# Optimization experiments

Measured on AMD Instinct MI355X. Metric: run time of the kernel, lower is better.

Reference implementation:

```python
import jax, jax.numpy as jnp
import numpy as np
from jax import lax

B, S, N, DIM = 4, 512, 16, 8
D_MODEL, D_STATE = 1024, 64
INPUT_SIZE = N * DIM
LN_EPS = 1e-5


def setup_inputs() -> dict:
    key = jax.random.key(0)
    ks = jax.random.split(key, 8)
    s = 0.02
    x = jax.random.normal(ks[0], (B, S, N, DIM), dtype=jnp.float32)
    W_emb = jax.random.normal(ks[1], (INPUT_SIZE, D_MODEL), dtype=jnp.float32) * s
    b_emb = jnp.zeros((D_MODEL,), jnp.float32)
    W_xp = jax.random.normal(ks[2], (D_MODEL, 2 * D_STATE + 1), dtype=jnp.float32) * s
    b_xp = jnp.zeros((2 * D_STATE + 1,), jnp.float32)
    # A init: -exp(arange(1, d_state+1) * 0.1), matching the torch module
    A = -jnp.exp(jnp.arange(1, D_STATE + 1, dtype=jnp.float32) * 0.1)
    Dp = jnp.ones((D_MODEL,), jnp.float32)
    gamma = jnp.ones((D_MODEL,), jnp.float32)
    beta = jnp.zeros((D_MODEL,), jnp.float32)
    W_out = jax.random.normal(ks[3], (D_MODEL, INPUT_SIZE), dtype=jnp.float32) * s
    b_out = jnp.zeros((INPUT_SIZE,), jnp.float32)
    return {"x": x, "W_emb": W_emb, "b_emb": b_emb, "W_xp": W_xp, "b_xp": b_xp,
            "A": A, "Dp": Dp, "gamma": gamma, "beta": beta,
            "W_out": W_out, "b_out": b_out}


def reference(x, W_emb, b_emb, W_xp, b_xp, A, Dp, gamma, beta, W_out, b_out):
    b, s, n, dim = x.shape
    d_state = A.shape[0]
    d_model = W_emb.shape[1]
    u = x.reshape(b, s, n * dim) @ W_emb + b_emb            # [B,S,dm]
    sel = u @ W_xp + b_xp                                    # [B,S,2*ds+1]
    delta = jax.nn.softplus(sel[..., 0:1]) * 0.01            # [B,S,1]
    Bs = sel[..., 1:1 + d_state]                             # [B,S,ds]
    Cs = sel[..., 1 + d_state:]                              # [B,S,ds]
    A_bar = jnp.exp(delta * A)                               # [B,S,ds]
    B_bar = delta * Bs                                       # [B,S,ds]

    def step(h, inp):
        a_t, b_t, c_t, u_t = inp                             # [B,ds],[B,ds],[B,ds],[B,dm]
        h = h * a_t[:, None, :] + b_t[:, None, :] * u_t[:, :, None]  # [B,dm,ds]
        y_t = jnp.einsum('bmd,bd->bm', h, c_t) + u_t * Dp
        return h, y_t

    h0 = jnp.zeros((b, d_model, d_state), x.dtype)
    xs = (jnp.swapaxes(A_bar, 0, 1), jnp.swapaxes(B_bar, 0, 1),
          jnp.swapaxes(Cs, 0, 1), jnp.swapaxes(u, 0, 1))
    _, ys = lax.scan(step, h0, xs)                           # ys: [S,B,dm]
    y = jnp.swapaxes(ys, 0, 1)                               # [B,S,dm]
    mu = y.mean(-1, keepdims=True)
    var = y.var(-1, keepdims=True)
    yn = (y - mu) / jnp.sqrt(var + LN_EPS) * gamma + beta
    pred = yn @ W_out + b_out                                # [B,S,N*D]
    return pred.reshape(b, s, n, dim)
```

## Files before the change

kernel.cpp:

```cpp
#include <hip/hip_runtime.h>
#include <cstddef>

typedef __attribute__((ext_vector_type(8))) short short8;
typedef __attribute__((ext_vector_type(4))) float f32x4;

constexpr int CL = 32;

__device__ inline ushort tobf(float f) {
  union { float f; unsigned u; } v; v.f = f;
  return (ushort)((v.u + 0x7FFFu + ((v.u >> 16) & 1u)) >> 16);
}
__device__ inline float frombf(ushort u) {
  union { unsigned u; float f; } v; v.u = ((unsigned)u) << 16; return v.f;
}

__global__ __launch_bounds__(256)
void prep(const float* __restrict__ Wemb, const float* __restrict__ Wxp,
          const float* __restrict__ Wout, const float* __restrict__ x,
          const float* __restrict__ bxp, const float* __restrict__ bout,
          ushort* __restrict__ WembT, ushort* __restrict__ wBCdT,
          ushort* __restrict__ WoutT, ushort* __restrict__ xbf,
          float* __restrict__ sel, float* __restrict__ sums,
          float* __restrict__ out) {
  int idx = blockIdx.x * 256 + threadIdx.x;
  if (idx < 131072) {
    int n = idx >> 7, k = idx & 127;
    WembT[idx] = tobf(Wemb[k * 1024 + n]);
  } else if (idx < 327680) {
    int j = idx - 131072;
    int n = j >> 10, k = j & 1023;
    float v = (n < 128) ? Wxp[k * 129 + 1 + n] : (n == 128 ? Wxp[k * 129] : 0.f);
    wBCdT[j] = tobf(v);
  } else if (idx < 458752) {
    int j = idx - 327680;
    int n = j >> 10, k = j & 1023;
    WoutT[j] = tobf(Wout[k * 128 + n]);
  } else if (idx < 720896) {
    int j = idx - 458752;
    xbf[j] = tobf(x[j]);
  } else if (idx < 1114112) {
    int j = idx - 720896;
    int c = j % 192;
    sel[j] = (c < 128) ? bxp[1 + c] : (c == 128 ? bxp[0] : 0.f);
  } else if (idx < 1118208) {
    sums[idx - 1114112] = 0.f;
  } else if (idx < 1380352) {
    int j = idx - 1118208;
    out[j] = bout[j & 127];
  }
}

template<int MODE>
__global__ __launch_bounds__(256)
void gemm_bt(const ushort* __restrict__ A, const ushort* __restrict__ BT,
             const float* __restrict__ bias, float* __restrict__ Cf,
             ushort* __restrict__ Cbf, int M, int N, int K, int kchunk) {
  __shared__ __align__(16) ushort sA[8192];
  __shared__ __align__(16) ushort sB[8192];
  const int t  = threadIdx.x;
  const int n0 = blockIdx.x * 64;
  const int m0 = blockIdx.y * 64;
  const int k0 = (MODE == 1) ? blockIdx.z * kchunk : 0;
  const int k1 = (MODE == 1) ? k0 + kchunk : K;

  const int lane = t & 63, w = t >> 6;
  const int wr = w << 4;
  const int colsel = lane & 15;
  const int kg = lane >> 4;

  f32x4 acc[4];
  #pragma unroll
  for (int nf = 0; nf < 4; ++nf) acc[nf] = (f32x4)(0.f);

  for (int kc = k0; kc < k1; kc += 128) {
    __syncthreads();
    #pragma unroll
    for (int i = 0; i < 4; ++i) {
      int c = t + (i << 8);
      int row = c >> 4, kk = (c & 15) << 3;
      float4 va  = *(const float4*)(A  + (size_t)(m0 + row) * K + kc + kk);
      float4 vb4 = *(const float4*)(BT + (size_t)(n0 + row) * K + kc + kk);
      int byteoff = ((row << 8) + (kk << 1)) ^ ((row & 7) << 4);
      *(float4*)((char*)sA + byteoff) = va;
      *(float4*)((char*)sB + byteoff) = vb4;
    }
    __syncthreads();
    short8 a[4];
    {
      int arow = wr + colsel;
      int lin = (arow << 8) + (kg << 4);
      int swz = (arow & 7) << 4;
      #pragma unroll
      for (int ks = 0; ks < 4; ++ks)
        a[ks] = *(const short8*)((const char*)sA + ((lin + (ks << 6)) ^ swz));
    }
    #pragma unroll
    for (int nf = 0; nf < 4; ++nf) {
      int brow = (nf << 4) + colsel;
      int lin = (brow << 8) + (kg << 4);
      int swz = (brow & 7) << 4;
      #pragma unroll
      for (int ks = 0; ks < 4; ++ks) {
        short8 b = *(const short8*)((const char*)sB + ((lin + (ks << 6)) ^ swz));
        acc[nf] = __builtin_amdgcn_mfma_f32_16x16x32_bf16(a[ks], b, acc[nf], 0, 0, 0);
      }
    }
  }
  const int r4 = kg << 2;
  #pragma unroll
  for (int nf = 0; nf < 4; ++nf) {
    int gn = n0 + (nf << 4) + colsel;
    #pragma unroll
    for (int reg = 0; reg < 4; ++reg) {
      int gm = m0 + wr + r4 + reg;
      if (MODE == 0) {
        Cbf[(size_t)gm * N + gn] = tobf(acc[nf][reg] + bias[gn]);
      } else {
        atomicAdd(&Cf[(size_t)gm * N + gn], acc[nf][reg]);
      }
    }
  }
}

__global__ __launch_bounds__(256)
void gemm_ln(const ushort* __restrict__ ybf, const ushort* __restrict__ BT,
             const float* __restrict__ sums, const float* __restrict__ gamma,
             const float* __restrict__ beta, float* __restrict__ out) {
  __shared__ __align__(16) ushort sA[8192];
  __shared__ __align__(16) ushort sB[8192];
  __shared__ float sLN[128];
  const int t  = threadIdx.x;
  const int n0 = blockIdx.x * 64;
  const int m0 = blockIdx.y * 64;
  const int k0 = blockIdx.z * 256;
  const int k1 = k0 + 256;

  if (t < 64) {
    float s1 = sums[m0 + t], s2 = sums[2048 + m0 + t];
    float mean = s1 * (1.f / 1024.f);
    float var  = s2 * (1.f / 1024.f) - mean * mean;
    sLN[2 * t] = mean;
    sLN[2 * t + 1] = rsqrtf(var + 1e-5f);
  }

  const int lane = t & 63, w = t >> 6;
  const int wr = w << 4;
  const int colsel = lane & 15;
  const int kg = lane >> 4;
  const int kk_t = (t & 15) << 3;

  f32x4 acc[4];
  #pragma unroll
  for (int nf = 0; nf < 4; ++nf) acc[nf] = (f32x4)(0.f);

  for (int kc = k0; kc < k1; kc += 128) {
    float4 g0 = *(const float4*)&gamma[kc + kk_t];
    float4 g1 = *(const float4*)&gamma[kc + kk_t + 4];
    float4 be0 = *(const float4*)&beta[kc + kk_t];
    float4 be1 = *(const float4*)&beta[kc + kk_t + 4];
    float gv[8] = {g0.x, g0.y, g0.z, g0.w, g1.x, g1.y, g1.z, g1.w};
    float bv[8] = {be0.x, be0.y, be0.z, be0.w, be1.x, be1.y, be1.z, be1.w};
    __syncthreads();
    #pragma unroll
    for (int i = 0; i < 4; ++i) {
      int c = t + (i << 8);
      int row = c >> 4, kk = (c & 15) << 3;
      short8 ya = *(const short8*)(ybf + (size_t)(m0 + row) * 1024 + kc + kk);
      float4 vb4 = *(const float4*)(BT + (size_t)(n0 + row) * 1024 + kc + kk);
      float mean = sLN[2 * row], rstd = sLN[2 * row + 1];
      short8 na;
      #pragma unroll
      for (int j = 0; j < 8; ++j) {
        float yv = frombf((ushort)ya[j]);
        na[j] = (short)tobf((yv - mean) * rstd * gv[j] + bv[j]);
      }
      int byteoff = ((row << 8) + (kk << 1)) ^ ((row & 7) << 4);
      *(short8*)((char*)sA + byteoff) = na;
      *(float4*)((char*)sB + byteoff) = vb4;
    }
    __syncthreads();
    short8 a[4];
    {
      int arow = wr + colsel;
      int lin = (arow << 8) + (kg << 4);
      int swz = (arow & 7) << 4;
      #pragma unroll
      for (int ks = 0; ks < 4; ++ks)
        a[ks] = *(const short8*)((const char*)sA + ((lin + (ks << 6)) ^ swz));
    }
    #pragma unroll
    for (int nf = 0; nf < 4; ++nf) {
      int brow = (nf << 4) + colsel;
      int lin = (brow << 8) + (kg << 4);
      int swz = (brow & 7) << 4;
      #pragma unroll
      for (int ks = 0; ks < 4; ++ks) {
        short8 b = *(const short8*)((const char*)sB + ((lin + (ks << 6)) ^ swz));
        acc[nf] = __builtin_amdgcn_mfma_f32_16x16x32_bf16(a[ks], b, acc[nf], 0, 0, 0);
      }
    }
  }
  const int r4 = kg << 2;
  #pragma unroll
  for (int nf = 0; nf < 4; ++nf) {
    int gn = n0 + (nf << 4) + colsel;
    #pragma unroll
    for (int reg = 0; reg < 4; ++reg) {
      int gm = m0 + wr + r4 + reg;
      atomicAdd(&out[(size_t)gm * 128 + gn], acc[nf][reg]);
    }
  }
}

__device__ __forceinline__ void transform_sbuf(float* sbuf, float a_d, int t) {
  const int d = t & 63;
  #pragma unroll
  for (int i = 0; i < 8; ++i) {
    float* R = sbuf + ((t >> 6) + i * 4) * 192;
    float draw = R[128];
    float sp = (draw > 15.f) ? draw : log1pf(__expf(draw));
    float delta = 0.01f * sp;
    R[d] = delta * R[d];
    R[128 + d] = __expf(delta * a_d);
  }
}

__global__ __launch_bounds__(256)
void scan_sum(const ushort* __restrict__ ubf, const float* __restrict__ sel,
              const float* __restrict__ A,
              float* __restrict__ cst, float* __restrict__ Ach) {
  __shared__ __align__(16) float sbuf[CL * 192];
  const int t = threadIdx.x, lane = t & 63, w = t >> 6;
  const int tc = blockIdx.x % 15;
  const int mg = (blockIdx.x / 15) & 3;
  const int b  = blockIdx.x / 60;
  const int r0 = b * 512 + tc * CL;

  const float a_d = A[t & 63];
  const float4* src = (const float4*)(sel + (size_t)r0 * 192);
  #pragma unroll
  for (int i = 0; i < 6; ++i)
    ((float4*)sbuf)[t + i * 256] = src[t + i * 256];
  __syncthreads();
  transform_sbuf(sbuf, a_d, t);
  __syncthreads();

  const int m = (mg * 4 + w) * 64 + lane;
  const ushort* ub = ubf + (size_t)r0 * 1024 + m;
  const bool doAp = (mg == 0 && w == 0);

  float2 h[32], ap[32];
  #pragma unroll
  for (int j = 0; j < 32; ++j) { h[j] = make_float2(0.f, 0.f); ap[j] = make_float2(1.f, 1.f); }

  float u0 = frombf(ub[0]);
  float u1 = frombf(ub[1024]);
  for (int s = 0; s < CL; ++s) {
    int sn = (s < CL - 3) ? s + 2 : CL - 1;
    float u2 = frombf(ub[(size_t)sn * 1024]);
    const float* L = sbuf + s * 192;
    #pragma unroll
    for (int jj = 0; jj < 16; ++jj) {
      float4 a4 = *(const float4*)&L[128 + 4 * jj];
      float4 b4 = *(const float4*)&L[4 * jj];
      h[2 * jj].x     = fmaf(h[2 * jj].x,     a4.x, b4.x * u0);
      h[2 * jj].y     = fmaf(h[2 * jj].y,     a4.y, b4.y * u0);
      h[2 * jj + 1].x = fmaf(h[2 * jj + 1].x, a4.z, b4.z * u0);
      h[2 * jj + 1].y = fmaf(h[2 * jj + 1].y, a4.w, b4.w * u0);
    }
    if (doAp) {
      #pragma unroll
      for (int jj = 0; jj < 16; ++jj) {
        float4 a4 = *(const float4*)&L[128 + 4 * jj];
        ap[2 * jj].x     *= a4.x;
        ap[2 * jj].y     *= a4.y;
        ap[2 * jj + 1].x *= a4.z;
        ap[2 * jj + 1].y *= a4.w;
      }
    }
    u0 = u1; u1 = u2;
  }

  size_t cbase = (((size_t)b * 15 + tc) * 64) * 1024 + m;
  #pragma unroll
  for (int j = 0; j < 32; ++j) {
    cst[cbase + (size_t)(2 * j)     * 1024] = h[j].x;
    cst[cbase + (size_t)(2 * j + 1) * 1024] = h[j].y;
  }
  if (doAp && lane == 0) {
    float2* ad = (float2*)&Ach[((size_t)b * 15 + tc) * 64];
    #pragma unroll
    for (int j = 0; j < 32; ++j) ad[j] = ap[j];
  }
}

__global__ __launch_bounds__(256)
void scan_comb(float* __restrict__ cst, const float* __restrict__ Ach) {
  int g = blockIdx.x * 256 + threadIdx.x;
  int b = g >> 16;
  int rem = g & 65535;
  int d = rem >> 10;
  int m = rem & 1023;
  float h = 0.f;
  for (int t2 = 0; t2 < 15; ++t2) {
    size_t idx = (((size_t)(b * 15 + t2)) * 64 + d) * 1024 + m;
    h = fmaf(Ach[(b * 15 + t2) * 64 + d], h, cst[idx]);
    cst[idx] = h;
  }
}

__global__ __launch_bounds__(256)
void scan_out(const ushort* __restrict__ ubf, const float* __restrict__ sel,
              const float* __restrict__ A, const float* __restrict__ cst,
              const float* __restrict__ Dp, ushort* __restrict__ ybf,
              float* __restrict__ sums) {
  __shared__ __align__(16) float sbuf[CL * 192];
  const int t = threadIdx.x, lane = t & 63, w = t >> 6;
  const int tc = blockIdx.x & 15;
  const int mg = (blockIdx.x >> 4) & 3;
  const int b  = blockIdx.x >> 6;
  const int r0 = b * 512 + tc * CL;

  const float a_d = A[t & 63];
  const float4* src = (const float4*)(sel + (size_t)r0 * 192);
  #pragma unroll
  for (int i = 0; i < 6; ++i)
    ((float4*)sbuf)[t + i * 256] = src[t + i * 256];
  __syncthreads();
  transform_sbuf(sbuf, a_d, t);
  __syncthreads();

  const int m = (mg * 4 + w) * 64 + lane;
  const ushort* ub = ubf + (size_t)r0 * 1024 + m;
  ushort* yb = ybf + (size_t)r0 * 1024 + m;
  const float dp = Dp[m];

  float2 h[32];
  if (tc == 0) {
    #pragma unroll
    for (int j = 0; j < 32; ++j) h[j] = make_float2(0.f, 0.f);
  } else {
    size_t cbase = (((size_t)b * 15 + (tc - 1)) * 64) * 1024 + m;
    #pragma unroll
    for (int j = 0; j < 32; ++j) {
      h[j].x = cst[cbase + (size_t)(2 * j)     * 1024];
      h[j].y = cst[cbase + (size_t)(2 * j + 1) * 1024];
    }
  }

  float u0 = frombf(ub[0]);
  float u1 = frombf(ub[1024]);
  for (int s = 0; s < CL; ++s) {
    int sn = (s < CL - 3) ? s + 2 : CL - 1;
    float u2 = frombf(ub[(size_t)sn * 1024]);
    const float* L = sbuf + s * 192;
    float y0 = 0.f, y1 = 0.f, y2 = 0.f, y3 = 0.f;
    #pragma unroll
    for (int jj = 0; jj < 16; ++jj) {
      float4 a4 = *(const float4*)&L[128 + 4 * jj];
      float4 b4 = *(const float4*)&L[4 * jj];
      float4 c4 = *(const float4*)&L[64 + 4 * jj];
      h[2 * jj].x     = fmaf(h[2 * jj].x,     a4.x, b4.x * u0);
      h[2 * jj].y     = fmaf(h[2 * jj].y,     a4.y, b4.y * u0);
      h[2 * jj + 1].x = fmaf(h[2 * jj + 1].x, a4.z, b4.z * u0);
      h[2 * jj + 1].y = fmaf(h[2 * jj + 1].y, a4.w, b4.w * u0);
      y0 = fmaf(c4.x, h[2 * jj].x,     y0);
      y1 = fmaf(c4.y, h[2 * jj].y,     y1);
      y2 = fmaf(c4.z, h[2 * jj + 1].x, y2);
      y3 = fmaf(c4.w, h[2 * jj + 1].y, y3);
    }
    float yv = (y0 + y1) + (y2 + y3) + u0 * dp;
    yb[(size_t)s * 1024] = tobf(yv);
    float rs1 = yv, rs2 = yv * yv;
    #pragma unroll
    for (int o = 32; o; o >>= 1) {
      rs1 += __shfl_xor(rs1, o, 64);
      rs2 += __shfl_xor(rs2, o, 64);
    }
    if (lane == 0) {
      atomicAdd(&sums[r0 + s], rs1);
      atomicAdd(&sums[2048 + r0 + s], rs2);
    }
    u0 = u1; u1 = u2;
  }
}

extern "C" void kernel_launch(void* const* d_in, const int* in_sizes, int n_in,
                              void* d_out, int out_size, void* d_ws, size_t ws_size,
                              hipStream_t stream) {
  const float* x     = (const float*)d_in[0];
  const float* Wemb  = (const float*)d_in[1];
  const float* bemb  = (const float*)d_in[2];
  const float* Wxp   = (const float*)d_in[3];
  const float* bxp   = (const float*)d_in[4];
  const float* A     = (const float*)d_in[5];
  const float* Dp    = (const float*)d_in[6];
  const float* gamma = (const float*)d_in[7];
  const float* beta  = (const float*)d_in[8];
  const float* Wout  = (const float*)d_in[9];
  const float* bout  = (const float*)d_in[10];
  float* out = (float*)d_out;
  float* ws  = (float*)d_ws;

  float* sel  = ws;
  float* cst  = ws + 393216;
  float* Ach  = ws + 4325376;
  float* sums = ws + 4329472;
  ushort* ubf   = (ushort*)(ws + 4333568);
  ushort* ybf   = ubf + 2097152;
  ushort* xbf   = ybf + 2097152;
  ushort* WembT = xbf + 262144;
  ushort* wBCdT = WembT + 131072;
  ushort* WoutT = wBCdT + 196608;

  prep<<<5392, 256, 0, stream>>>(Wemb, Wxp, Wout, x, bxp, bout,
                                 WembT, wBCdT, WoutT, xbf, sel, sums, out);
  gemm_bt<0><<<dim3(16, 32, 1), 256, 0, stream>>>(
      xbf, WembT, bemb, nullptr, ubf, 2048, 1024, 128, 0);
  gemm_bt<1><<<dim3(3, 32, 4), 256, 0, stream>>>(
      ubf, wBCdT, nullptr, sel, nullptr, 2048, 192, 1024, 256);
  scan_sum<<<240, 256, 0, stream>>>(ubf, sel, A, cst, Ach);
  scan_comb<<<1024, 256, 0, stream>>>(cst, Ach);
  scan_out<<<256, 256, 0, stream>>>(ubf, sel, A, cst, Dp, ybf, sums);
  gemm_ln<<<dim3(2, 32, 4), 256, 0, stream>>>(
      ybf, WoutT, sums, gamma, beta, out);
}
```

Measured before the change: 186.3 us.

## Halve scan chunk length to double chunk parallelism and batch LN row-sum reductions

```diff
diff --git a/kernel.cpp b/kernel.cpp
--- a/kernel.cpp
+++ b/kernel.cpp
@@ -4,7 +4,9 @@
 typedef __attribute__((ext_vector_type(8))) short short8;
 typedef __attribute__((ext_vector_type(4))) float f32x4;
 
-constexpr int CL = 32;
+constexpr int CL  = 16;
+constexpr int NTC = 32;
+constexpr int NC1 = 31;
 
 __device__ inline ushort tobf(float f) {
   union { float f; unsigned u; } v; v.f = f;
@@ -215,7 +217,7 @@
 __device__ __forceinline__ void transform_sbuf(float* sbuf, float a_d, int t) {
   const int d = t & 63;
   #pragma unroll
-  for (int i = 0; i < 8; ++i) {
+  for (int i = 0; i < 4; ++i) {
     float* R = sbuf + ((t >> 6) + i * 4) * 192;
     float draw = R[128];
     float sp = (draw > 15.f) ? draw : log1pf(__expf(draw));
@@ -231,15 +233,15 @@
               float* __restrict__ cst, float* __restrict__ Ach) {
   __shared__ __align__(16) float sbuf[CL * 192];
   const int t = threadIdx.x, lane = t & 63, w = t >> 6;
-  const int tc = blockIdx.x % 15;
-  const int mg = (blockIdx.x / 15) & 3;
-  const int b  = blockIdx.x / 60;
+  const int tc = blockIdx.x % NC1;
+  const int mg = (blockIdx.x / NC1) & 3;
+  const int b  = blockIdx.x / (NC1 * 4);
   const int r0 = b * 512 + tc * CL;
 
   const float a_d = A[t & 63];
   const float4* src = (const float4*)(sel + (size_t)r0 * 192);
   #pragma unroll
-  for (int i = 0; i < 6; ++i)
+  for (int i = 0; i < 3; ++i)
     ((float4*)sbuf)[t + i * 256] = src[t + i * 256];
   __syncthreads();
   transform_sbuf(sbuf, a_d, t);
@@ -281,14 +283,14 @@
     u0 = u1; u1 = u2;
   }
 
-  size_t cbase = (((size_t)b * 15 + tc) * 64) * 1024 + m;
+  size_t cbase = (((size_t)b * NC1 + tc) * 64) * 1024 + m;
   #pragma unroll
   for (int j = 0; j < 32; ++j) {
     cst[cbase + (size_t)(2 * j)     * 1024] = h[j].x;
     cst[cbase + (size_t)(2 * j + 1) * 1024] = h[j].y;
   }
   if (doAp && lane == 0) {
-    float2* ad = (float2*)&Ach[((size_t)b * 15 + tc) * 64];
+    float2* ad = (float2*)&Ach[((size_t)b * NC1 + tc) * 64];
     #pragma unroll
     for (int j = 0; j < 32; ++j) ad[j] = ap[j];
   }
@@ -302,9 +304,9 @@
   int d = rem >> 10;
   int m = rem & 1023;
   float h = 0.f;
-  for (int t2 = 0; t2 < 15; ++t2) {
-    size_t idx = (((size_t)(b * 15 + t2)) * 64 + d) * 1024 + m;
-    h = fmaf(Ach[(b * 15 + t2) * 64 + d], h, cst[idx]);
+  for (int t2 = 0; t2 < NC1; ++t2) {
+    size_t idx = (((size_t)(b * NC1 + t2)) * 64 + d) * 1024 + m;
+    h = fmaf(Ach[(b * NC1 + t2) * 64 + d], h, cst[idx]);
     cst[idx] = h;
   }
 }
@@ -315,16 +317,17 @@
               const float* __restrict__ Dp, ushort* __restrict__ ybf,
               float* __restrict__ sums) {
   __shared__ __align__(16) float sbuf[CL * 192];
+  __shared__ float y_lds[256 * 17];
   const int t = threadIdx.x, lane = t & 63, w = t >> 6;
-  const int tc = blockIdx.x & 15;
-  const int mg = (blockIdx.x >> 4) & 3;
-  const int b  = blockIdx.x >> 6;
+  const int tc = blockIdx.x & 31;
+  const int mg = (blockIdx.x >> 5) & 3;
+  const int b  = blockIdx.x >> 7;
   const int r0 = b * 512 + tc * CL;
 
   const float a_d = A[t & 63];
   const float4* src = (const float4*)(sel + (size_t)r0 * 192);
   #pragma unroll
-  for (int i = 0; i < 6; ++i)
+  for (int i = 0; i < 3; ++i)
     ((float4*)sbuf)[t + i * 256] = src[t + i * 256];
   __syncthreads();
   transform_sbuf(sbuf, a_d, t);
@@ -340,7 +343,7 @@
     #pragma unroll
     for (int j = 0; j < 32; ++j) h[j] = make_float2(0.f, 0.f);
   } else {
-    size_t cbase = (((size_t)b * 15 + (tc - 1)) * 64) * 1024 + m;
+    size_t cbase = (((size_t)b * NC1 + (tc - 1)) * 64) * 1024 + m;
     #pragma unroll
     for (int j = 0; j < 32; ++j) {
       h[j].x = cst[cbase + (size_t)(2 * j)     * 1024];
@@ -371,17 +374,28 @@
     }
     float yv = (y0 + y1) + (y2 + y3) + u0 * dp;
     yb[(size_t)s * 1024] = tobf(yv);
-    float rs1 = yv, rs2 = yv * yv;
+    y_lds[t * 17 + s] = yv;
+    u0 = u1; u1 = u2;
+  }
+  __syncthreads();
+  #pragma unroll
+  for (int rr = 0; rr < 4; ++rr) {
+    int s = w * 4 + rr;
+    float s1 = 0.f, s2 = 0.f;
+    #pragma unroll
+    for (int i = 0; i < 4; ++i) {
+      float v = y_lds[(i * 64 + lane) * 17 + s];
+      s1 += v; s2 += v * v;
+    }
     #pragma unroll
     for (int o = 32; o; o >>= 1) {
-      rs1 += __shfl_xor(rs1, o, 64);
-      rs2 += __shfl_xor(rs2, o, 64);
+      s1 += __shfl_xor(s1, o, 64);
+      s2 += __shfl_xor(s2, o, 64);
     }
     if (lane == 0) {
-      atomicAdd(&sums[r0 + s], rs1);
-      atomicAdd(&sums[2048 + r0 + s], rs2);
-    }
-    u0 = u1; u1 = u2;
+      atomicAdd(&sums[r0 + s], s1);
+      atomicAdd(&sums[2048 + r0 + s], s2);
+    }
   }
 }
 
@@ -404,9 +418,9 @@
 
   float* sel  = ws;
   float* cst  = ws + 393216;
-  float* Ach  = ws + 4325376;
-  float* sums = ws + 4329472;
-  ushort* ubf   = (ushort*)(ws + 4333568);
+  float* Ach  = ws + 8519680;
+  float* sums = ws + 8527872;
+  ushort* ubf   = (ushort*)(ws + 8531968);
   ushort* ybf   = ubf + 2097152;
   ushort* xbf   = ybf + 2097152;
   ushort* WembT = xbf + 262144;
@@ -419,9 +433,9 @@
       xbf, WembT, bemb, nullptr, ubf, 2048, 1024, 128, 0);
   gemm_bt<1><<<dim3(3, 32, 4), 256, 0, stream>>>(
       ubf, wBCdT, nullptr, sel, nullptr, 2048, 192, 1024, 256);
-  scan_sum<<<240, 256, 0, stream>>>(ubf, sel, A, cst, Ach);
+  scan_sum<<<4 * NC1 * 4, 256, 0, stream>>>(ubf, sel, A, cst, Ach);
   scan_comb<<<1024, 256, 0, stream>>>(cst, Ach);
-  scan_out<<<256, 256, 0, stream>>>(ubf, sel, A, cst, Dp, ybf, sums);
+  scan_out<<<512, 256, 0, stream>>>(ubf, sel, A, cst, Dp, ybf, sums);
   gemm_ln<<<dim3(2, 32, 4), 256, 0, stream>>>(
       ybf, WoutT, sums, gamma, beta, out);
 }
```

New measurement: 165.6 us. -11.1%, faster.
